# Kernel optimization log

Hardware: AMD Instinct MI355X
Metric: run time of the kernel (lower is better)

Reference implementation:

```python
import jax, jax.numpy as jnp
import numpy as np

S = 768    # sequence length (residues)
CS = 384   # single_embedding_size
CP = 128   # pair_embedding_size
E = 16     # embedding_size per head
PQ = 4     # num_query_points
PV = 8     # num_value_points
H = 12     # num_heads


def setup_inputs() -> dict:
    key = jax.random.key(0)
    ks = jax.random.split(key, 14)

    def w(k, shape, scale=0.02):
        return jax.random.normal(k, shape, dtype=jnp.float32) * scale

    # Orthonormal rotation matrices per residue (proper rigid frames)
    rot_raw = jax.random.normal(ks[2], (S, 3, 3), dtype=jnp.float32)
    rotations, _ = jnp.linalg.qr(rot_raw)

    return {
        "single_representation": jax.random.normal(ks[0], (S, CS), dtype=jnp.float32),
        "pair_representation": jax.random.normal(ks[1], (S, S, CP), dtype=jnp.float32),
        "frames_rotations": rotations,
        "frames_translations": jax.random.normal(ks[3], (S, 3), dtype=jnp.float32),
        # learned parameters (layouts match the torch view() conventions)
        "Wq": w(ks[4], (H, E, CS)),
        "Wk": w(ks[5], (H, E, CS)),
        "Wv": w(ks[6], (H, E, CS)),
        "Wqp": w(ks[7], (H, PQ, 3, CS)),
        "Wkp": w(ks[8], (H, PQ, 3, CS)),
        "Wvp": w(ks[9], (H, PV, 3, CS)),
        "Wb": w(ks[10], (H, CP)),
        "Wo": w(ks[11], (CS, H * (CP + E + PV * 4))),
        "bo": jnp.zeros((CS,), dtype=jnp.float32),
        "gamma": jnp.ones((H,), dtype=jnp.float32),  # scale_head parameter
    }


def _frame_apply(R, t, x):
    # R: [S,3,3], t: [S,3], x: [H,S,P,3] -> R_s @ x + t_s per residue s
    return jnp.einsum('sij,hspj->hspi', R, x) + t[None, :, None, :]


def reference(single_representation, pair_representation, frames_rotations,
              frames_translations, Wq, Wk, Wv, Wqp, Wkp, Wvp, Wb, Wo, bo, gamma):
    s_len = single_representation.shape[0]
    e = Wq.shape[1]
    pq = Wqp.shape[1]
    scale_single = 1.0 / np.sqrt(e)
    scale_frame = -1.0 / np.sqrt(18.0 * pq)

    # --- attention logits from three sources ---
    q = jnp.einsum('hec,sc->hse', Wq, single_representation)
    k = jnp.einsum('hec,sc->hse', Wk, single_representation)
    w_single = scale_single * jnp.einsum('hie,hje->hij', q, k)          # [H,S,S]

    w_pair = jnp.einsum('hc,ijc->hij', Wb, pair_representation)          # [H,S,S]

    qp = jnp.einsum('hpdc,sc->hspd', Wqp, single_representation)         # [H,S,PQ,3]
    kp = jnp.einsum('hpdc,sc->hspd', Wkp, single_representation)
    lqp = _frame_apply(frames_rotations, frames_translations, qp)
    lkp = _frame_apply(frames_rotations, frames_translations, kp)
    diff = lqp[:, :, None, :, :] - lkp[:, None, :, :, :]                 # [H,S,S,PQ,3]
    w_frame = jnp.sum(diff * diff, axis=(-2, -1))                        # [H,S,S]
    w_frame = scale_frame * jax.nn.softplus(gamma)[:, None, None] * w_frame

    a = jax.nn.softmax(w_single + w_pair + w_frame, axis=-1)             # [H,S,S]

    # --- fan-out into three attention outputs ---
    v = jnp.einsum('hec,sc->hse', Wv, single_representation)
    o_single = jnp.einsum('hij,hje->ihe', a, v).reshape(s_len, -1)       # [S, H*E]

    # faithful to source: sum over the query dim of a, then contract keys
    a_sum = jnp.sum(a, axis=1)                                           # [H,S(keys)]
    o_pair = jnp.einsum('hk,ikc->ihc', a_sum, pair_representation).reshape(s_len, -1)

    vp = jnp.einsum('hpdc,sc->hspd', Wvp, single_representation)         # [H,S,PV,3]
    lvp = _frame_apply(frames_rotations, frames_translations, vp)
    o_local = jnp.einsum('hij,hjpd->hipd', a, lvp)                       # [H,S,PV,3]
    Rinv = jnp.swapaxes(frames_rotations, -1, -2)
    tinv = -jnp.einsum('sij,sj->si', Rinv, frames_translations)
    o_global = _frame_apply(Rinv, tinv, o_local)                         # [H,S,PV,3]
    o_pts = jnp.transpose(o_global, (1, 2, 0, 3)).reshape(s_len, -1)     # [S, PV*H*3]
    o_norm = jnp.transpose(jnp.linalg.norm(o_global, axis=-1), (1, 2, 0)).reshape(s_len, -1)

    attn = jnp.concatenate([o_single, o_pair, o_pts, o_norm], axis=-1)
    return attn @ Wo.T + bo
```

## Files before the change

### kernel.cpp

```cpp
#include <hip/hip_runtime.h>
#include <hip/hip_bf16.h>

#define S 768
#define CS 384
#define CP 128
#define E 16
#define PQ 4
#define PV 8
#define H 12
#define FDIM 2112
#define OFF_PAIR 192
#define OFF_PTS 1728
#define OFF_NORM 2016

typedef __hip_bfloat16 bf16;

__device__ __forceinline__ float b2f(bf16 x){ return __bfloat162float(x); }
__device__ __forceinline__ bf16 f2b(float x){ return __float2bfloat16(x); }
__device__ __forceinline__ float blo(unsigned u){ return __uint_as_float(u << 16); }
__device__ __forceinline__ float bhi(unsigned u){ return __uint_as_float(u & 0xffff0000u); }
__device__ __forceinline__ unsigned pk2(float a, float b){
  bf16 x = f2b(a), y = f2b(b);
  unsigned short ux = *reinterpret_cast<unsigned short*>(&x);
  unsigned short uy = *reinterpret_cast<unsigned short*>(&y);
  return (unsigned)ux | ((unsigned)uy << 16);
}

__global__ __launch_bounds__(256) void k_proj_wpair(
    const float* __restrict__ sr, const float* __restrict__ rot, const float* __restrict__ trans,
    const float* __restrict__ Wq, const float* __restrict__ Wk, const float* __restrict__ Wv,
    const float* __restrict__ Wqp, const float* __restrict__ Wkp, const float* __restrict__ Wvp,
    float* __restrict__ q, float* __restrict__ kT, unsigned* __restrict__ vf2,
    float* __restrict__ lqp, float* __restrict__ lkpT,
    const float* __restrict__ pair, const float* __restrict__ Wb, float* __restrict__ wp)
{
  if (blockIdx.x < S/2){
    int s0 = blockIdx.x*2;
    if (threadIdx.x < 96){
      int hh = threadIdx.x >> 3, c = 40 + (threadIdx.x & 7);
      vf2[((size_t)hh*(S/2) + blockIdx.x)*48 + c] = 0u;
    }
    __shared__ float srs[2][CS];
    __shared__ float Rs[2][9];
    __shared__ float ts[2][3];
    for (int x = threadIdx.x; x < 2*CS; x += 256) ((float*)srs)[x] = sr[(size_t)s0*CS + x];
    if (threadIdx.x < 18) ((float*)Rs)[threadIdx.x] = rot[(size_t)s0*9 + threadIdx.x];
    if (threadIdx.x >= 64 && threadIdx.x < 70) ((float*)ts)[threadIdx.x-64] = trans[(size_t)s0*3 + threadIdx.x-64];
    __syncthreads();

    for (int task = threadIdx.x; task < 768; task += 256){
      if (task < 576){
        int which = task / 192;
        int he = task - which*192;
        int h = he >> 4, e = he & 15;
        const float* W = (which==0 ? Wq : (which==1 ? Wk : Wv)) + (size_t)he*CS;
        const float4* W4 = (const float4*)W;
        float acc[2] = {0.f,0.f};
        for (int cc = 0; cc < CS/4; ++cc){
          float4 w = W4[cc];
          #pragma unroll
          for (int r = 0; r < 2; ++r){
            const float* sp = srs[r] + cc*4;
            acc[r] += w.x*sp[0] + w.y*sp[1] + w.z*sp[2] + w.w*sp[3];
          }
        }
        if (which == 0){
          #pragma unroll
          for (int r = 0; r < 2; ++r) q[((size_t)h*S + s0+r)*E + e] = acc[r];
        } else if (which == 1){
          #pragma unroll
          for (int r = 0; r < 2; ++r) kT[((size_t)h*E + e)*S + s0+r] = acc[r];
        } else {
          vf2[((size_t)h*(S/2) + (s0>>1))*48 + e] = pk2(acc[0], acc[1]);
        }
      } else {
        int pt = task - 576;
        int h = pt >> 4, slot = pt & 15;
        int kind, p; const float* W;
        if (slot < 4)      { kind = 0; p = slot;     W = Wqp + (size_t)((h*PQ+p)*3)*CS; }
        else if (slot < 8) { kind = 1; p = slot - 4; W = Wkp + (size_t)((h*PQ+p)*3)*CS; }
        else               { kind = 2; p = slot - 8; W = Wvp + (size_t)((h*PV+p)*3)*CS; }
        const float4* W0 = (const float4*)W;
        const float4* W1 = (const float4*)(W + CS);
        const float4* W2 = (const float4*)(W + 2*CS);
        float a0[2] = {0,0}, a1[2] = {0,0}, a2[2] = {0,0};
        for (int cc = 0; cc < CS/4; ++cc){
          float4 w0 = W0[cc], w1 = W1[cc], w2 = W2[cc];
          #pragma unroll
          for (int r = 0; r < 2; ++r){
            const float* sp = srs[r] + cc*4;
            a0[r] += w0.x*sp[0] + w0.y*sp[1] + w0.z*sp[2] + w0.w*sp[3];
            a1[r] += w1.x*sp[0] + w1.y*sp[1] + w1.z*sp[2] + w1.w*sp[3];
            a2[r] += w2.x*sp[0] + w2.y*sp[1] + w2.z*sp[2] + w2.w*sp[3];
          }
        }
        float lv[2][3];
        #pragma unroll
        for (int r = 0; r < 2; ++r){
          int s = s0 + r;
          float l0 = Rs[r][0]*a0[r] + Rs[r][1]*a1[r] + Rs[r][2]*a2[r] + ts[r][0];
          float l1 = Rs[r][3]*a0[r] + Rs[r][4]*a1[r] + Rs[r][5]*a2[r] + ts[r][1];
          float l2 = Rs[r][6]*a0[r] + Rs[r][7]*a1[r] + Rs[r][8]*a2[r] + ts[r][2];
          if (kind == 0){ float* d = lqp + ((size_t)h*S + s)*12 + p*3; d[0]=l0; d[1]=l1; d[2]=l2; }
          else if (kind == 1){
            float* dst = lkpT + (size_t)h*12*S;
            dst[(size_t)(p*3+0)*S + s] = l0;
            dst[(size_t)(p*3+1)*S + s] = l1;
            dst[(size_t)(p*3+2)*S + s] = l2;
          } else {
            lv[r][0]=l0; lv[r][1]=l1; lv[r][2]=l2;
          }
        }
        if (kind == 2){
          size_t base = ((size_t)h*(S/2) + (s0>>1))*48 + 16 + p*3;
          vf2[base+0] = pk2(lv[0][0], lv[1][0]);
          vf2[base+1] = pk2(lv[0][1], lv[1][1]);
          vf2[base+2] = pk2(lv[0][2], lv[1][2]);
        }
      }
    }
  } else {
    int r = (blockIdx.x - S/2)*256 + threadIdx.x;
    const float4* prow = (const float4*)(pair + (size_t)r*CP);
    float acc[H];
    #pragma unroll
    for (int h = 0; h < H; ++h) acc[h] = 0.f;
    #pragma unroll
    for (int half = 0; half < 2; ++half){
      float4 buf[16];
      #pragma unroll
      for (int cc = 0; cc < 16; ++cc) buf[cc] = prow[half*16 + cc];
      #pragma unroll
      for (int h = 0; h < H; ++h){
        const float4* wb = (const float4*)(Wb + h*CP + half*64);
        float p0=0.f, p1=0.f, p2=0.f, p3=0.f;
        #pragma unroll
        for (int cc = 0; cc < 16; ++cc){
          float4 wv = wb[cc];
          p0 += wv.x*buf[cc].x; p1 += wv.y*buf[cc].y;
          p2 += wv.z*buf[cc].z; p3 += wv.w*buf[cc].w;
        }
        acc[h] += (p0+p1)+(p2+p3);
      }
    }
    #pragma unroll
    for (int h = 0; h < H; ++h) wp[(size_t)h*S*S + r] = acc[h];
  }
}

__global__ __launch_bounds__(256) void k_attn(
    const float* __restrict__ wp,
    const float* __restrict__ q, const float* __restrict__ kT,
    const float* __restrict__ lqp, const float* __restrict__ lkpT,
    const float* __restrict__ gamma, bf16* __restrict__ ab)
{
  int i    = blockIdx.x / 3;
  int hg   = blockIdx.x % 3;
  int lane = threadIdx.x & 63;
  int w    = __builtin_amdgcn_readfirstlane(threadIdx.x >> 6);
  int h    = hg*4 + w;

  __shared__ float lgs[4][S];

  const float* qrow = q   + ((size_t)h*S + i)*E;
  const float* lqr  = lqp + ((size_t)h*S + i)*12;
  const float* wrow = wp  + ((size_t)h*S + i)*S;
  const float* kTh  = kT   + (size_t)h*E*S;
  const float* lkTh = lkpT + (size_t)h*12*S;
  float sf = -0.11785113019775793f * log1pf(__expf(gamma[h]));

  float qv[E];
  #pragma unroll
  for (int e = 0; e < E; ++e) qv[e] = qrow[e];
  float lq[12];
  #pragma unroll
  for (int x = 0; x < 12; ++x) lq[x] = lqr[x];

  float mloc = -1e30f;
  #pragma unroll 2
  for (int jj = 0; jj < 12; ++jj){
    int j = lane + jj*64;
    float d = 0.f;
    #pragma unroll
    for (int e = 0; e < E; ++e) d += qv[e]*kTh[(size_t)e*S + j];
    float fr = 0.f;
    #pragma unroll
    for (int x = 0; x < 12; ++x){ float df = lq[x] - lkTh[(size_t)x*S + j]; fr += df*df; }
    float lg = wrow[j] + 0.25f*d + sf*fr;
    lgs[w][j] = lg;
    mloc = fmaxf(mloc, lg);
  }
  #pragma unroll
  for (int mk = 1; mk < 64; mk <<= 1) mloc = fmaxf(mloc, __shfl_xor(mloc, mk));

  float sum = 0.f;
  #pragma unroll 3
  for (int jj = 0; jj < 12; ++jj){
    int j = lane + jj*64;
    float v = __expf(lgs[w][j] - mloc);
    lgs[w][j] = v;
    sum += v;
  }
  #pragma unroll
  for (int mk = 1; mk < 64; mk <<= 1) sum += __shfl_xor(sum, mk);
  float inv = 1.f/sum;

  size_t base = ((size_t)h*S + i)*S;
  #pragma unroll 3
  for (int jj = 0; jj < 12; ++jj){
    int j = lane + jj*64;
    ab[base + j] = f2b(lgs[w][j]*inv);
  }
}

__global__ __launch_bounds__(256) void k_sv_asum(
    const bf16* __restrict__ ab, const unsigned* __restrict__ vf2,
    const float* __restrict__ rot, const float* __restrict__ trans,
    bf16* __restrict__ attnb, float* __restrict__ asumT)
{
  if (blockIdx.x < 384){
    int h  = blockIdx.x / 32;
    int i0 = (blockIdx.x % 32) * 24;
    int t  = threadIdx.x;
    float a0 = 0.f, a1 = 0.f, a2 = 0.f;
    for (int i = i0; i < i0 + 24; ++i){
      const bf16* row = ab + ((size_t)h*S + i)*S;
      a0 += b2f(row[t]);
      a1 += b2f(row[t + 256]);
      a2 += b2f(row[t + 512]);
    }
    atomicAdd(&asumT[(t      )*H + h], a0);
    atomicAdd(&asumT[(t + 256)*H + h], a1);
    atomicAdd(&asumT[(t + 512)*H + h], a2);
  } else {
    int bid  = blockIdx.x - 384;
    int h    = bid / (S/4);
    int i0   = (bid % (S/4))*4;
    int w    = threadIdx.x >> 6;
    int lane = threadIdx.x & 63;
    int i = i0 + w;
    const unsigned* arow = (const unsigned*)(ab + ((size_t)h*S + i)*S);
    float acc = 0.f;
    if (lane < 48){
      const unsigned* vrow = vf2 + (size_t)h*(S/2)*48 + lane;
      float acc1 = 0.f;
      #pragma unroll 4
      for (int jp = 0; jp < S/2; jp += 2){
        unsigned ap0 = arow[jp], ap1 = arow[jp+1];
        unsigned vp0 = vrow[(size_t)jp*48], vp1 = vrow[(size_t)(jp+1)*48];
        acc  += blo(ap0)*blo(vp0) + bhi(ap0)*bhi(vp0);
        acc1 += blo(ap1)*blo(vp1) + bhi(ap1)*bhi(vp1);
      }
      acc += acc1;
    }
    __shared__ float ol[4][24];
    __shared__ float ogs[4][24];
    int pd = lane - 16;
    if (lane >= 16 && lane < 40) ol[w][pd] = acc;
    __syncthreads();
    if (lane < 16){
      attnb[(size_t)i*FDIM + h*E + lane] = f2b(acc);
    } else if (lane < 40){
      int p = pd/3, d = pd%3;
      float r0 = rot[(size_t)i*9 + 0 + d];
      float r1 = rot[(size_t)i*9 + 3 + d];
      float r2 = rot[(size_t)i*9 + 6 + d];
      float x0 = ol[w][p*3+0] - trans[i*3+0];
      float x1 = ol[w][p*3+1] - trans[i*3+1];
      float x2 = ol[w][p*3+2] - trans[i*3+2];
      float og = r0*x0 + r1*x1 + r2*x2;
      attnb[(size_t)i*FDIM + OFF_PTS + p*(H*3) + h*3 + d] = f2b(og);
      ogs[w][pd] = og;
    }
    __syncthreads();
    if (lane >= 16 && lane < 40 && (pd % 3) == 0){
      int p = pd/3;
      float g0 = ogs[w][p*3], g1 = ogs[w][p*3+1], g2 = ogs[w][p*3+2];
      attnb[(size_t)i*FDIM + OFF_NORM + p*H + h] = f2b(sqrtf(g0*g0 + g1*g1 + g2*g2));
    }
  }
}

__global__ __launch_bounds__(512) void k_opair(const float* __restrict__ pair,
                                               const float* __restrict__ asumT,
                                               bf16* __restrict__ attnb)
{
  int i  = blockIdx.x;
  int t  = threadIdx.x;
  int c2 = t & 63;
  int g  = __builtin_amdgcn_readfirstlane(t >> 6);
  float accx[H], accy[H];
  #pragma unroll
  for (int h = 0; h < H; ++h){ accx[h] = 0.f; accy[h] = 0.f; }
  const float2* prow = (const float2*)(pair + (size_t)i*S*CP) + c2;
  for (int kk = 0; kk < 96; ++kk){
    int kj = g*96 + kk;
    float2 pv = prow[(size_t)kj*64];
    const float* ap = asumT + kj*H;
    #pragma unroll
    for (int h = 0; h < H; ++h){
      accx[h] += ap[h]*pv.x;
      accy[h] += ap[h]*pv.y;
    }
  }
  __shared__ float part[8][H][CP];
  #pragma unroll
  for (int h = 0; h < H; ++h)
    ((float2*)part[g][h])[c2] = make_float2(accx[h], accy[h]);
  __syncthreads();
  if (t < CP){
    #pragma unroll
    for (int h = 0; h < H; ++h){
      float s = part[0][h][t] + part[1][h][t] + part[2][h][t] + part[3][h][t]
              + part[4][h][t] + part[5][h][t] + part[6][h][t] + part[7][h][t];
      attnb[(size_t)i*FDIM + OFF_PAIR + h*CP + t] = f2b(s);
    }
  }
}

__global__ __launch_bounds__(384) void k_final(const bf16* __restrict__ attnb,
                                               const float* __restrict__ Wo,
                                               const float* __restrict__ bo,
                                               float* __restrict__ out)
{
  int i0 = blockIdx.x*4;
  int ck = blockIdx.y;
  int o  = threadIdx.x;
  const float4* wrow = (const float4*)(Wo + (size_t)o*FDIM) + ck*132;
  const unsigned* a0 = (const unsigned*)(attnb + (size_t)i0*FDIM) + ck*264;
  const unsigned* a1 = a0 + FDIM/2;
  const unsigned* a2 = a1 + FDIM/2;
  const unsigned* a3 = a2 + FDIM/2;
  float c0=0.f, c1=0.f, c2=0.f, c3=0.f;
  for (int cc = 0; cc < 132; ++cc){
    float4 wv = wrow[cc];
    unsigned u;
    u = a0[cc*2]; c0 += wv.x*blo(u)+wv.y*bhi(u); u = a0[cc*2+1]; c0 += wv.z*blo(u)+wv.w*bhi(u);
    u = a1[cc*2]; c1 += wv.x*blo(u)+wv.y*bhi(u); u = a1[cc*2+1]; c1 += wv.z*blo(u)+wv.w*bhi(u);
    u = a2[cc*2]; c2 += wv.x*blo(u)+wv.y*bhi(u); u = a2[cc*2+1]; c2 += wv.z*blo(u)+wv.w*bhi(u);
    u = a3[cc*2]; c3 += wv.x*blo(u)+wv.y*bhi(u); u = a3[cc*2+1]; c3 += wv.z*blo(u)+wv.w*bhi(u);
  }
  if (ck == 0){
    float b = bo[o];
    c0 += b; c1 += b; c2 += b; c3 += b;
  }
  atomicAdd(&out[(size_t)(i0+0)*CS + o], c0);
  atomicAdd(&out[(size_t)(i0+1)*CS + o], c1);
  atomicAdd(&out[(size_t)(i0+2)*CS + o], c2);
  atomicAdd(&out[(size_t)(i0+3)*CS + o], c3);
}

extern "C" void kernel_launch(void* const* d_in, const int* in_sizes, int n_in,
                              void* d_out, int out_size, void* d_ws, size_t ws_size,
                              hipStream_t stream)
{
  const float* sr    = (const float*)d_in[0];
  const float* pair  = (const float*)d_in[1];
  const float* rot   = (const float*)d_in[2];
  const float* trans = (const float*)d_in[3];
  const float* Wq    = (const float*)d_in[4];
  const float* Wk    = (const float*)d_in[5];
  const float* Wv    = (const float*)d_in[6];
  const float* Wqp   = (const float*)d_in[7];
  const float* Wkp   = (const float*)d_in[8];
  const float* Wvp   = (const float*)d_in[9];
  const float* Wb    = (const float*)d_in[10];
  const float* Wo    = (const float*)d_in[11];
  const float* bo    = (const float*)d_in[12];
  const float* gamma = (const float*)d_in[13];

  float* ws    = (float*)d_ws;
  float*    q     = ws;
  float*    kT    = q    + 147456;
  float*    lqp   = kT   + 147456;
  float*    lkpT  = lqp  + 110592;
  unsigned* vf2   = (unsigned*)(lkpT + 110592);
  float*    asumT = (float*)(vf2 + 221184);
  bf16*     ab    = (bf16*)(asumT + 9216);
  bf16*     attnb = (bf16*)(asumT + 9216 + 3538944);
  float*    wp    = asumT + 9216 + 3538944 + 811008;
  float* out = (float*)d_out;

  hipMemsetAsync(asumT, 0, (size_t)S*H*sizeof(float), stream);
  hipMemsetAsync(out,   0, (size_t)S*CS*sizeof(float), stream);
  k_proj_wpair<<<S/2 + (S*S)/256, 256, 0, stream>>>(sr, rot, trans, Wq, Wk, Wv, Wqp, Wkp, Wvp,
                                                    q, kT, vf2, lqp, lkpT, pair, Wb, wp);
  k_attn      <<<S*3,             256, 0, stream>>>(wp, q, kT, lqp, lkpT, gamma, ab);
  k_sv_asum   <<<384 + H*(S/4),   256, 0, stream>>>(ab, vf2, rot, trans, attnb, asumT);
  k_opair     <<<S,               512, 0, stream>>>(pair, asumT, attnb);
  k_final     <<<dim3(S/4, 4),    384, 0, stream>>>(attnb, Wo, bo, out);
}
```

Measured before the change: 750.8 us.

## Stage pair rows through swizzled LDS ring buffer for coalesced w_pair projection

Rewrites the pair-bias projection branch. Each block now streams 8-row chunks of the pair tensor into a triple-buffered, XOR-swizzled LDS ring using fully coalesced 16-byte loads, replacing the old per-thread strided 512-byte row reads. Each wave computes three heads, keeping its Wb slice in registers, and reduces partial dot products with cross-lane shuffles. Results are staged in LDS and then written out coalesced. The cost is a barrier per chunk plus hand-written waitcnt/barrier sequencing that could be fragile.

```diff
diff --git a/kernel.cpp b/kernel.cpp
--- a/kernel.cpp
+++ b/kernel.cpp
@@ -34,15 +34,17 @@
     float* __restrict__ lqp, float* __restrict__ lkpT,
     const float* __restrict__ pair, const float* __restrict__ Wb, float* __restrict__ wp)
 {
+  __shared__ __align__(16) float lds_all[6144];
+
   if (blockIdx.x < S/2){
+    float (*srs)[CS] = (float(*)[CS])lds_all;
+    float (*Rs)[9]   = (float(*)[9])(lds_all + 768);
+    float (*ts)[3]   = (float(*)[3])(lds_all + 786);
     int s0 = blockIdx.x*2;
     if (threadIdx.x < 96){
       int hh = threadIdx.x >> 3, c = 40 + (threadIdx.x & 7);
       vf2[((size_t)hh*(S/2) + blockIdx.x)*48 + c] = 0u;
     }
-    __shared__ float srs[2][CS];
-    __shared__ float Rs[2][9];
-    __shared__ float ts[2][3];
     for (int x = threadIdx.x; x < 2*CS; x += 256) ((float*)srs)[x] = sr[(size_t)s0*CS + x];
     if (threadIdx.x < 18) ((float*)Rs)[threadIdx.x] = rot[(size_t)s0*9 + threadIdx.x];
     if (threadIdx.x >= 64 && threadIdx.x < 70) ((float*)ts)[threadIdx.x-64] = trans[(size_t)s0*3 + threadIdx.x-64];
@@ -120,31 +122,80 @@
       }
     }
   } else {
-    int r = (blockIdx.x - S/2)*256 + threadIdx.x;
-    const float4* prow = (const float4*)(pair + (size_t)r*CP);
-    float acc[H];
-    #pragma unroll
-    for (int h = 0; h < H; ++h) acc[h] = 0.f;
-    #pragma unroll
-    for (int half = 0; half < 2; ++half){
-      float4 buf[16];
+    int bwp = blockIdx.x - S/2;
+    size_t rowBase = (size_t)bwp * 256;
+    int t    = threadIdx.x;
+    int lane = t & 63;
+    int hg   = __builtin_amdgcn_readfirstlane(t >> 6);
+    int r    = lane & 7;
+    int cg   = (lane >> 3) & 7;
+
+    const float4* Wb4 = (const float4*)Wb;
+    float4 wb0[4], wb1[4], wb2[4];
+    #pragma unroll
+    for (int u = 0; u < 4; ++u){
+      wb0[u] = Wb4[(hg*3+0)*32 + cg*4 + u];
+      wb1[u] = Wb4[(hg*3+1)*32 + cg*4 + u];
+      wb2[u] = Wb4[(hg*3+2)*32 + cg*4 + u];
+    }
+
+    int rs   = t >> 5;
+    int slot = t & 31;
+    int sw   = slot ^ rs;
+    float* outw = lds_all + 3072;
+    const uint4* psrc = (const uint4*)pair;
+
+    uint4 rA = psrc[(rowBase + rs)*32 + slot];
+    uint4 rB = psrc[(rowBase + 8 + rs)*32 + slot];
+    *((float4*)(lds_all) + rs*32 + sw) = *(float4*)&rA;
+
+    auto COMPUTE = [&](int c, int b){
+      const float4* ch4 = (const float4*)(lds_all + b*1024);
+      float a0 = 0.f, a1 = 0.f, a2 = 0.f;
+      int rb32 = r*32, cb = cg*4;
       #pragma unroll
-      for (int cc = 0; cc < 16; ++cc) buf[cc] = prow[half*16 + cc];
-      #pragma unroll
-      for (int h = 0; h < H; ++h){
-        const float4* wb = (const float4*)(Wb + h*CP + half*64);
-        float p0=0.f, p1=0.f, p2=0.f, p3=0.f;
-        #pragma unroll
-        for (int cc = 0; cc < 16; ++cc){
-          float4 wv = wb[cc];
-          p0 += wv.x*buf[cc].x; p1 += wv.y*buf[cc].y;
-          p2 += wv.z*buf[cc].z; p3 += wv.w*buf[cc].w;
-        }
-        acc[h] += (p0+p1)+(p2+p3);
-      }
-    }
-    #pragma unroll
-    for (int h = 0; h < H; ++h) wp[(size_t)h*S*S + r] = acc[h];
+      for (int u = 0; u < 4; ++u){
+        float4 p = ch4[rb32 + ((cb+u) ^ r)];
+        a0 += wb0[u].x*p.x + wb0[u].y*p.y + wb0[u].z*p.z + wb0[u].w*p.w;
+        a1 += wb1[u].x*p.x + wb1[u].y*p.y + wb1[u].z*p.z + wb1[u].w*p.w;
+        a2 += wb2[u].x*p.x + wb2[u].y*p.y + wb2[u].z*p.z + wb2[u].w*p.w;
+      }
+      a0 += __shfl_xor(a0, 8); a0 += __shfl_xor(a0, 16); a0 += __shfl_xor(a0, 32);
+      a1 += __shfl_xor(a1, 8); a1 += __shfl_xor(a1, 16); a1 += __shfl_xor(a1, 32);
+      a2 += __shfl_xor(a2, 8); a2 += __shfl_xor(a2, 16); a2 += __shfl_xor(a2, 32);
+      if (cg == 0){
+        int row = c*8 + r;
+        outw[(hg*3+0)*256 + row] = a0;
+        outw[(hg*3+1)*256 + row] = a1;
+        outw[(hg*3+2)*256 + row] = a2;
+      }
+    };
+
+    for (int cc = 0; cc < 16; ++cc){
+      int c0 = cc*2, c1 = cc*2 + 1;
+      if (c0+2 < 32) rA = psrc[(rowBase + (size_t)(c0+2)*8 + rs)*32 + slot];
+      {
+        int bw = (c0+1)%3;
+        *((float4*)(lds_all + bw*1024) + rs*32 + sw) = *(float4*)&rB;
+      }
+      asm volatile("s_waitcnt lgkmcnt(0)" ::: "memory");
+      __builtin_amdgcn_s_barrier();
+      asm volatile("" ::: "memory");
+      COMPUTE(c0, c0%3);
+      if (c1+2 < 32) rB = psrc[(rowBase + (size_t)(c1+2)*8 + rs)*32 + slot];
+      if (c1+1 < 32){
+        int bw = (c1+1)%3;
+        *((float4*)(lds_all + bw*1024) + rs*32 + sw) = *(float4*)&rA;
+      }
+      asm volatile("s_waitcnt lgkmcnt(0)" ::: "memory");
+      __builtin_amdgcn_s_barrier();
+      asm volatile("" ::: "memory");
+      COMPUTE(c1, c1%3);
+    }
+    __syncthreads();
+    #pragma unroll
+    for (int x = 0; x < 12; ++x)
+      wp[(size_t)x*S*S + rowBase + t] = outw[x*256 + t];
   }
 }
 
```

New measurement: 755.7 us. Within noise of the previous version (+0.7%).
